# Kernel optimization log

Measured on AMD Instinct MI355X. Metric: run time of the kernel, lower is better.

Reference implementation:

```python
import jax, jax.numpy as jnp
import numpy as np

B, N, E, D, L, NC = 64, 128, 1024, 256, 2, 7
BETA = 0.3  # args.diffloss
BIG = 1e30  # mask_logic constant (score - (1-adj)*1e30), as in torch source lineage


def setup_inputs():
    key = jax.random.key(0)
    ks = iter(jax.random.split(key, 48))
    def p(shape, s=0.02):
        return jax.random.normal(next(ks), shape, jnp.float32) * s
    inp = {}
    inp["features"] = jax.random.normal(next(ks), (B, N, E), jnp.float32)
    inp["adj_1"] = jax.random.randint(next(ks), (B, N, N), 0, 2, jnp.int32)
    inp["adj_2"] = jax.random.randint(next(ks), (B, N, N), 0, 2, jnp.int32)
    inp["s_mask"] = jax.random.randint(next(ks), (B, N, N), 0, 2, jnp.int32)
    inp["s_mask_onehot"] = jnp.zeros((B, N, N, 2), jnp.int32)
    inp["lengths"] = jnp.full((B,), N, jnp.int32)
    inp["fc1_w"] = p((D, E)); inp["fc1_b"] = jnp.zeros((D,), jnp.float32)
    # GRUCell params (torch layout: weight_ih (3D,D) order r,z,n)
    for nm in ["gcs", "gps", "gcl", "gpl"]:
        inp[nm + "_wih"] = p((L, 3 * D, D)); inp[nm + "_whh"] = p((L, 3 * D, D))
        inp[nm + "_bih"] = jnp.zeros((L, 3 * D), jnp.float32)
        inp[nm + "_bhh"] = jnp.zeros((L, 3 * D), jnp.float32)
    # GatDot params per layer: linear1 (Q proj), linear2 (K proj)
    for nm in ["gats", "gatl"]:
        inp[nm + "_wq"] = p((L, D, D)); inp[nm + "_bq"] = jnp.zeros((L, D), jnp.float32)
        inp[nm + "_wk"] = p((L, D, D)); inp[nm + "_bk"] = jnp.zeros((L, D), jnp.float32)
    inp["affine1"] = p((2 * D, 2 * D), 0.05)
    inp["affine2"] = p((2 * D, 2 * D), 0.05)
    IN = 4 * D + E  # hidden*2*2 + emb_dim
    inp["mlp_w1"] = p((D, IN)); inp["mlp_b1"] = jnp.zeros((D,), jnp.float32)
    inp["mlp_w2"] = p((D, D)); inp["mlp_b2"] = jnp.zeros((D,), jnp.float32)
    inp["out_w"] = p((NC, D)); inp["out_b"] = jnp.zeros((NC,), jnp.float32)
    return inp


def gru_cell(x, h, wih, whh, bih, bhh):
    gi = x @ wih.T + bih
    gh = h @ whh.T + bhh
    ir, iz, in_ = jnp.split(gi, 3, axis=-1)
    hr, hz, hn = jnp.split(gh, 3, axis=-1)
    r = jax.nn.sigmoid(ir + hr)
    z = jax.nn.sigmoid(iz + hz)
    n = jnp.tanh(in_ + r * hn)
    return (1.0 - z) * n + z * h


def dag_pass(H_in, adj, gat, cpar, ppar):
    """Sequential DAG pass: per-utterance masked dot-product gather + GRU-C/GRU-P."""
    wq, bq, wk, bk = gat
    n = H_in.shape[1]
    idx = jnp.arange(n)

    def step(carry, inp):
        H1, Kb = carry            # H1: [B,N,D] written prefix; Kb = linear2(H1)
        i, x, arow = inp          # x: [B,D], arow: [B,N]
        q = x @ wq.T + bq
        scores = jnp.einsum('bnd,bd->bn', Kb, q)
        # torch: alpha - (1-adj)*1e30 over prefix :i; positions >= i excluded
        logits = scores - (1.0 - arow) * BIG - (idx >= i).astype(scores.dtype) * (2.0 * BIG)
        w = jax.nn.softmax(logits, axis=-1)
        M = jnp.einsum('bn,bnd->bd', w, H1)  # exactly 0 at i==0 (buffer zeros)
        C = gru_cell(x, M, *cpar)   # grus_c(input=x, hidden=M)
        P = gru_cell(M, x, *ppar)   # grus_p(input=M, hidden=x)
        h = C + P
        H1 = jax.lax.dynamic_update_slice(H1, h[:, None, :], (0, i, 0))
        Kb = jax.lax.dynamic_update_slice(Kb, (h @ wk.T + bk)[:, None, :], (0, i, 0))
        return (H1, Kb), None

    init = (jnp.zeros_like(H_in), jnp.zeros_like(H_in))
    xs = (idx, jnp.swapaxes(H_in, 0, 1), jnp.swapaxes(adj, 0, 1))
    (H1, _), _ = jax.lax.scan(step, init, xs)
    return H1


def diff_loss_fn(a, b):
    # orthogonality (DSN-style) loss between short/long channel features
    x = a.reshape(-1, a.shape[-1])
    y = b.reshape(-1, b.shape[-1])
    x = x - x.mean(axis=0, keepdims=True)
    y = y - y.mean(axis=0, keepdims=True)
    x = x / (jnp.linalg.norm(x, axis=1, keepdims=True) + 1e-6)
    y = y / (jnp.linalg.norm(y, axis=1, keepdims=True) + 1e-6)
    return jnp.mean((x.T @ y) ** 2)


def _forward(features, adj_1, adj_2,
             fc1_w, fc1_b,
             gcs_wih, gcs_whh, gcs_bih, gcs_bhh,
             gps_wih, gps_whh, gps_bih, gps_bhh,
             gcl_wih, gcl_whh, gcl_bih, gcl_bhh,
             gpl_wih, gpl_whh, gpl_bih, gpl_bhh,
             gats_wq, gats_bq, gats_wk, gats_bk,
             gatl_wq, gatl_bq, gatl_wk, gatl_bk,
             affine1, affine2,
             mlp_w1, mlp_b1, mlp_w2, mlp_b2, out_w, out_b):
    adj1 = adj_1.astype(jnp.float32)
    adj2 = adj_2.astype(jnp.float32)
    H0 = jax.nn.relu(features @ fc1_w.T + fc1_b)
    H0r = jax.nn.relu(features[:, ::-1] @ fc1_w.T + fc1_b)
    adj1r = adj1[:, ::-1, ::-1]
    adj2r = adj2[:, ::-1, ::-1]

    def channel(adjf, adjb, wq, bq, wk, bk, cwih, cwhh, cbih, cbhh, pwih, pwhh, pbih, pbhh):
        Hf, Hb = H0, H0r
        outs = []
        for l in range(L):
            gat = (wq[l], bq[l], wk[l], bk[l])
            cp = (cwih[l], cwhh[l], cbih[l], cbhh[l])
            pp = (pwih[l], pwhh[l], pbih[l], pbhh[l])
            Hf = dag_pass(Hf, adjf, gat, cp, pp)
            Hb = dag_pass(Hb, adjb, gat, cp, pp)
            outs.append(jnp.concatenate([Hf, Hb], axis=-1))  # no flip-back (as in source)
        return outs

    cs = channel(adj1, adj1r, gats_wq, gats_bq, gats_wk, gats_bk,
                 gcs_wih, gcs_whh, gcs_bih, gcs_bhh, gps_wih, gps_whh, gps_bih, gps_bhh)
    cl = channel(adj2, adj2r, gatl_wq, gatl_bq, gatl_wk, gatl_bk,
                 gcl_wih, gcl_whh, gcl_bih, gcl_bhh, gpl_wih, gpl_whh, gpl_bih, gpl_bhh)

    dloss = sum(diff_loss_fn(a, b) for a, b in zip(cs, cl)) * BETA

    HS, HL = cs[-1], cl[-1]  # [B,N,2D]
    A1 = jax.nn.softmax(jnp.einsum('bnd,de,bme->bnm', HS, affine1, HL), axis=-1)
    A2 = jax.nn.softmax(jnp.einsum('bnd,de,bme->bnm', HL, affine2, HS), axis=-1)
    HSn = jnp.einsum('bnm,bmd->bnd', A1, HL)
    HLn = jnp.einsum('bnm,bmd->bnd', A2, HS)

    Hfin = jnp.concatenate([features, HSn, HLn], axis=-1)  # in_dim = emb + 4D
    h = jax.nn.relu(Hfin @ mlp_w1.T + mlp_b1)
    h = jax.nn.relu(h @ mlp_w2.T + mlp_b2)
    logits = h @ out_w.T + out_b
    return logits, dloss


def reference(features, adj_1, adj_2, s_mask, s_mask_onehot, lengths,
              fc1_w, fc1_b,
              gcs_wih, gcs_whh, gcs_bih, gcs_bhh,
              gps_wih, gps_whh, gps_bih, gps_bhh,
              gcl_wih, gcl_whh, gcl_bih, gcl_bhh,
              gpl_wih, gpl_whh, gpl_bih, gpl_bhh,
              gats_wq, gats_bq, gats_wk, gats_bk,
              gatl_wq, gatl_bq, gatl_wk, gatl_bk,
              affine1, affine2,
              mlp_w1, mlp_b1, mlp_w2, mlp_b2, out_w, out_b):
    # s_mask / s_mask_onehot / lengths unused for attn_type='dotprod', no_rel_attn=True, nodal_att_type=None
    return _forward(features, adj_1, adj_2,
                    fc1_w, fc1_b,
                    gcs_wih, gcs_whh, gcs_bih, gcs_bhh,
                    gps_wih, gps_whh, gps_bih, gps_bhh,
                    gcl_wih, gcl_whh, gcl_bih, gcl_bhh,
                    gpl_wih, gpl_whh, gpl_bih, gpl_bhh,
                    gats_wq, gats_bq, gats_wk, gats_bk,
                    gatl_wq, gatl_bq, gatl_wk, gatl_bk,
                    affine1, affine2,
                    mlp_w1, mlp_b1, mlp_w2, mlp_b2, out_w, out_b)
```

## Files before the change

### kernel.cpp

```cpp
#include <hip/hip_runtime.h>
#include <hip/hip_fp16.h>
#include <math.h>

#define SB   64
#define SN   128
#define SE   1024
#define SD   256
#define SD2  512
#define SD3  768
#define SIN  2048
#define SNC  7
#define SBN  8192
#define CS   16

#define L_HS   0
#define L_GK   65536
#define L_XH   114688
#define L_QH   122880
#define L_MH   131072
#define L_LG   131584
#define L_WGT  132096
#define L_ADJ  132608
#define SMEM_BYTES 133120

typedef _Float16 h2v __attribute__((ext_vector_type(2)));

__device__ __forceinline__ float wsum(float v){
#pragma unroll
  for (int o = 32; o; o >>= 1) v += __shfl_xor(v, o);
  return v;
}
__device__ __forceinline__ float sigm(float x){ return 1.f/(1.f + expf(-x)); }

__device__ __forceinline__ unsigned short f2h(float f){
  return __half_as_ushort(__float2half_rn(f));
}
__device__ __forceinline__ float h2f_(unsigned short u){
  return __half2float(__ushort_as_half(u));
}
__device__ __forceinline__ h2v u2h(unsigned u){
  union { unsigned u; h2v h; } c; c.u = u; return c.h;
}
__device__ __forceinline__ float dot8d(uint4 w, uint4 m, float acc){
  acc = __builtin_amdgcn_fdot2(u2h(w.x), u2h(m.x), acc, false);
  acc = __builtin_amdgcn_fdot2(u2h(w.y), u2h(m.y), acc, false);
  acc = __builtin_amdgcn_fdot2(u2h(w.z), u2h(m.z), acc, false);
  acc = __builtin_amdgcn_fdot2(u2h(w.w), u2h(m.w), acc, false);
  return acc;
}

template<bool BKMAJ, bool BIAS, bool RELU, bool ACC>
__global__ __launch_bounds__(256)
void gemm_k(const float* __restrict__ A, const float* __restrict__ Bm,
            const float* __restrict__ bias, float* __restrict__ C,
            int Nn, int K, int lda, int ldb, int ldc,
            long sA, long sB, long sC)
// ... 74 lines not shown
  for (int p = 0; p < 6; ++p) {
    const int r = t + 256 * p;
    const float* src = (r < 768) ? (a.wc[cd] + (long)r * SD)
                                 : (a.wp[cd] + (long)(r - 768) * SD);
    const float4 v0 = *(const float4*)(src + kb8 * 8);
    const float4 v1 = *(const float4*)(src + kb8 * 8 + 4);
    uint4 o;
    o.x = (unsigned)f2h(v0.x) | ((unsigned)f2h(v0.y) << 16);
    o.y = (unsigned)f2h(v0.z) | ((unsigned)f2h(v0.w) << 16);
    o.z = (unsigned)f2h(v1.x) | ((unsigned)f2h(v1.y) << 16);
    o.w = (unsigned)f2h(v1.z) | ((unsigned)f2h(v1.w) << 16);
    *(uint4*)(a.Wt + (((size_t)cd * 32 + kb8) * 1536 + r) * 8) = o;
  }
}

__global__ void s0_k(const float* __restrict__ Q, const float* __restrict__ bk,
                     float* __restrict__ S0)
{
  const int r = blockIdx.x * 4 + (threadIdx.x >> 6), lane = threadIdx.x & 63;
  const float4 q  = *(const float4*)(Q + (long)r * SD + lane * 4);
  const float4 kb = *(const float4*)(bk + lane * 4);
  float p = q.x*kb.x + q.y*kb.y + q.z*kb.z + q.w*kb.w;
  p = wsum(p);
  if (lane == 0) S0[r] = p;
}

struct StepArgs {
  const float* Qt[4]; const float* S0[4];
  const int* adj[4]; int rev[4];
  const float* bc[4];  const float* bp[4];
  const float* bgc[4]; const float* bgp[4];
  const float* X[4];
  float* H1[4];
  unsigned short* Hh;
  const unsigned short* Wt;
  const unsigned short* Wgk;
  int ldX, s0;
};
__global__ __launch_bounds__(256, 1) void step_chunk_k(StepArgs a)
{
  extern __shared__ __align__(16) char dsm[];
  unsigned short* Hs_l = (unsigned short*)(dsm + L_HS);
  unsigned short* GKh  = (unsigned short*)(dsm + L_GK);
  unsigned short* Xh   = (unsigned short*)(dsm + L_XH);
  unsigned short* Qh   = (unsigned short*)(dsm + L_QH);
  unsigned short* Mh   = (unsigned short*)(dsm + L_MH);
  float* lg   = (float*)(dsm + L_LG);
  float* wgt  = (float*)(dsm + L_WGT);
  float* adjm = (float*)(dsm + L_ADJ);

  const int blk = blockIdx.x;
  const int cd = blk & 3, b = blk >> 2;
  const int t = threadIdx.x, q = t >> 6, l = t & 63;
  const int j = t;
  const int ldX = a.ldX, s0 = a.s0;
  const float* Xp  = a.X[cd];
  float* H1 = a.H1[cd];
  unsigned short* Hg = a.Hh + ((size_t)(cd * 64 + b)) * 128 * 256;
  const float* Qtp = a.Qt[cd];
  const float* S0p = a.S0[cd];
  const int*   adjp = a.adj[cd];
  const int    rev  = a.rev[cd];

  const float bc0 = a.bc[cd][j],  bc1 = a.bc[cd][256+j],  bc2 = a.bc[cd][512+j];
  const float bp0 = a.bp[cd][j],  bp1 = a.bp[cd][256+j],  bp2 = a.bp[cd][512+j];

#pragma unroll
  for (int s = 0; s < CS; ++s) {
    Xh[s*256 + t] = f2h(Xp[((long)(s0+s)*64 + b)*ldX + t]);
    Qh[s*256 + t] = f2h(Qtp[((long)(s0+s)*64 + b)*SD + t]);
  }
  for (int o = t*16; o < s0*512; o += 4096) {
    const uint4 v = *(const uint4*)((const char*)Hg + o);
    const int row = o >> 9, d2 = o & 511;
    *(uint4*)((char*)Hs_l + row*512 + (d2 ^ ((row & 7) << 4))) = v;
  }
  __syncthreads();

  {
    float gacc[6][CS];
#pragma unroll
    for (int g = 0; g < 6; ++g)
#pragma unroll
      for (int s = 0; s < CS; ++s) gacc[g][s] = 0.f;
    const unsigned short* wbase = a.Wgk + ((size_t)cd*32*1536 + j)*8;
    for (int kb8 = 0; kb8 < 32; ++kb8) {
      const uint4* wr = (const uint4*)(wbase + (size_t)kb8*12288);
      uint4 w[6];
#pragma unroll
      for (int g = 0; g < 6; ++g) w[g] = wr[g*256];
#pragma unroll
      for (int s = 0; s < CS; ++s) {
        const uint4 x8 = *(const uint4*)&Xh[s*256 + kb8*8];
#pragma unroll
        for (int g = 0; g < 6; ++g)
          gacc[g][s] = dot8d(w[g], x8, gacc[g][s]);
      }
    }
#pragma unroll
    for (int g = 0; g < 6; ++g) {
      const float bg = (g < 3) ? a.bgc[cd][g*256 + j] : a.bgp[cd][(g-3)*256 + j];
#pragma unroll
      for (int s = 0; s < CS; ++s)
        GKh[s*1536 + g*256 + j] = f2h(gacc[g][s] + bg);
    }
  }
  __syncthreads();

  for (int i = s0; i < s0 + CS; ++i) {
    float mreg;
    if (i == 0) {
      Mh[t] = 0;
      mreg = 0.f;
      __syncthreads();
    } else {
      if (t >= 128) {
        const int r = t - 128;
        const int ii = rev ? (SN-1-i) : i;
        const int nn = rev ? (SN-1-r) : r;
        adjm[r] = (float)adjp[((long)b*SN + ii)*SN + nn];
      } else {
        const int n = q*64 + l;
        const char* hrow = (const char*)Hs_l + n*512;
        const int c = (n & 7) << 4;
        const unsigned short* qrow = Qh + (i - s0)*256;
        float acc = 0.f;
#pragma unroll
        for (int k = 0; k < 32; ++k) {
          const uint4 hv = *(const uint4*)(hrow + ((k*16) ^ c));
          const uint4 qv = *(const uint4*)(qrow + k*8);
          acc = dot8d(hv, qv, acc);
        }
        lg[n] = acc;
      }
      __syncthreads();
      if (q == 0) {
        const float s0v = S0p[i*64 + b];
        const float v0 = (l < i)    ? (lg[l]    + s0v - (1.f - adjm[l]   )*1e30f) : -3.0e38f;
        const float v1 = (l+64 < i) ? (lg[l+64] + s0v - (1.f - adjm[l+64])*1e30f) : -3.0e38f;
        float mx = fmaxf(v0, v1);
#pragma unroll
        for (int o = 32; o; o >>= 1) mx = fmaxf(mx, __shfl_xor(mx, o));
        const float e0 = (l < i)    ? expf(v0 - mx) : 0.f;
        const float e1 = (l+64 < i) ? expf(v1 - mx) : 0.f;
        float sum = e0 + e1;
#pragma unroll
        for (int o = 32; o; o >>= 1) sum += __shfl_xor(sum, o);
        const float inv = 1.f / sum;
        if (l < i)    wgt[l]    = e0 * inv;
        if (l+64 < i) wgt[l+64] = e1 * inv;
      }
      __syncthreads();
      float m0 = 0.f, m1 = 0.f, m2 = 0.f, m3 = 0.f;
      int n = 0;
      for (; n + 8 <= i; n += 8) {
        m0 = fmaf(wgt[n+0], h2f_(Hs_l[(n+0)*256 + (j ^  0)]), m0);
        m1 = fmaf(wgt[n+1], h2f_(Hs_l[(n+1)*256 + (j ^  8)]), m1);
        m2 = fmaf(wgt[n+2], h2f_(Hs_l[(n+2)*256 + (j ^ 16)]), m2);
        m3 = fmaf(wgt[n+3], h2f_(Hs_l[(n+3)*256 + (j ^ 24)]), m3);
        m0 = fmaf(wgt[n+4], h2f_(Hs_l[(n+4)*256 + (j ^ 32)]), m0);
        m1 = fmaf(wgt[n+5], h2f_(Hs_l[(n+5)*256 + (j ^ 40)]), m1);
        m2 = fmaf(wgt[n+6], h2f_(Hs_l[(n+6)*256 + (j ^ 48)]), m2);
        m3 = fmaf(wgt[n+7], h2f_(Hs_l[(n+7)*256 + (j ^ 56)]), m3);
      }
      for (; n < i; ++n)
        m0 = fmaf(wgt[n], h2f_(Hs_l[n*256 + (j ^ ((n & 7) << 3))]), m0);
      mreg = (m0 + m1) + (m2 + m3);
      Mh[t] = f2h(mreg);
      __syncthreads();
    }

    float g0 = 0.f, g1 = 0.f, g2 = 0.f, g3 = 0.f, g4 = 0.f, g5 = 0.f;
    {
      const unsigned short* wb = a.Wt + ((size_t)cd*32*1536 + j)*8;
      const uint4* wr0 = (const uint4*)wb;
      uint4 c0 = wr0[0], c1 = wr0[256], c2 = wr0[512],
            c3 = wr0[768], c4 = wr0[1024], c5 = wr0[1280];
#pragma unroll 4
      for (int kb8 = 0; kb8 < 32; ++kb8) {
        uint4 n0 = c0, n1 = c1, n2 = c2, n3 = c3, n4 = c4, n5 = c5;
        if (kb8 < 31) {
          const uint4* wn = (const uint4*)(wb + (size_t)(kb8+1)*12288);
          n0 = wn[0]; n1 = wn[256]; n2 = wn[512];
          n3 = wn[768]; n4 = wn[1024]; n5 = wn[1280];
        }
        const uint4 m8 = *(const uint4*)&Mh[kb8*8];
        g0 = dot8d(c0, m8, g0);
        g1 = dot8d(c1, m8, g1);
        g2 = dot8d(c2, m8, g2);
        g3 = dot8d(c3, m8, g3);
        g4 = dot8d(c4, m8, g4);
        g5 = dot8d(c5, m8, g5);
        c0 = n0; c1 = n1; c2 = n2; c3 = n3; c4 = n4; c5 = n5;
      }
    }
    {
      const int sb = (i - s0)*1536;
      const float gic_r = h2f_(GKh[sb + j]);
      const float gic_z = h2f_(GKh[sb + 256 + j]);
      const float gic_n = h2f_(GKh[sb + 512 + j]);
      const float ghp_r = h2f_(GKh[sb + 768 + j]);
      const float ghp_z = h2f_(GKh[sb + 1024 + j]);
      const float ghp_n = h2f_(GKh[sb + 1280 + j]);
      const float xj = Xp[((long)i*64 + b)*ldX + j];
      const float rC = sigm(gic_r + g0 + bc0);
      const float zC = sigm(gic_z + g1 + bc1);
      const float nC = tanhf(gic_n + rC * (g2 + bc2));
      const float Cc = (1.f - zC) * nC + zC * mreg;
      const float rP = sigm(g3 + bp0 + ghp_r);
      const float zP = sigm(g4 + bp1 + ghp_z);
      const float nP = tanhf(g5 + bp2 + rP * ghp_n);
      const float hval = Cc + (1.f - zP) * nP + zP * xj;
      H1[((long)i*64 + b)*SD2 + j] = hval;
      const unsigned short hh = f2h(hval);
      Hs_l[i*256 + (j ^ ((i & 7) << 3))] = hh;
      Hg[(size_t)i*256 + j] = hh;
    }
    __syncthreads();
  }
}

__global__ void zero_k(float* p, long n)
{
  for (long idx = (long)blockIdx.x * 256 + threadIdx.x; idx < n; idx += (long)gridDim.x * 256)
    p[idx] = 0.f;
}

__global__ void colmean_k(const float* __restrict__ X, float* __restrict__ mean)
{
  __shared__ float red[256];
  const int c = blockIdx.x * 64 + (threadIdx.x & 63), rq = threadIdx.x >> 6;
  const int r0 = blockIdx.y * 256;
  float acc = 0.f;
  for (int r = r0 + rq; r < r0 + 256; r += 4) acc += X[(long)r * SD2 + c];
  red[threadIdx.x] = acc;
  __syncthreads();
  if (threadIdx.x < 64) {
    const float s = red[threadIdx.x] + red[64 + threadIdx.x] + red[128 + threadIdx.x] + red[192 + threadIdx.x];
    atomicAdd(&mean[c], s * (1.f / 8192.f));
  }
}

__global__ void rownorm_k(const float* __restrict__ X, const float* __restrict__ mean,
                          float* __restrict__ inv)
{
  const int r = blockIdx.x * 4 + (threadIdx.x >> 6), lane = threadIdx.x & 63;
  const float* xp = X + (long)r * SD2 + lane * 8;
  const float4 v0 = *(const float4*)xp;
  const float4 v1 = *(const float4*)(xp + 4);
  const float4 m0 = *(const float4*)(mean + lane * 8);
  const float4 m1 = *(const float4*)(mean + lane * 8 + 4);
// ... 83 lines not shown
#pragma unroll
  for (int o = 32; o; o >>= 1) s += __shfl_xor(s, o);
  const float inv = 1.f / s;
  p[lane] = e0 * inv; p[lane + 64] = e1 * inv;
}

__global__ void head_k(const float* __restrict__ H, const float* __restrict__ W,
                       const float* __restrict__ bo, float* __restrict__ out)
{
  const int r = blockIdx.x * 4 + (threadIdx.x >> 6), lane = threadIdx.x & 63;
  const float4 h = *(const float4*)(H + (long)r * SD + lane * 4);
#pragma unroll
  for (int c = 0; c < SNC; ++c) {
    const float4 w = *(const float4*)(W + (long)c * SD + lane * 4);
    float p = h.x*w.x + h.y*w.y + h.z*w.z + h.w*w.w;
    p = wsum(p);
    if (lane == 0) out[(long)r * SNC + c] = p + bo[c];
  }
}

__global__ void fin_k(const float* __restrict__ dl, float* __restrict__ out)
{
  out[0] = (dl[0] + dl[1]) * (0.3f / (512.f * 512.f));
}

extern "C" void kernel_launch(void* const* d_in, const int* in_sizes, int n_in,
                              void* d_out, int out_size, void* d_ws, size_t ws_size,
                              hipStream_t stream)
{
  (void)in_sizes; (void)n_in; (void)out_size; (void)ws_size;

  static bool attr_set = false;
  if (!attr_set) {
    hipFuncSetAttribute(reinterpret_cast<const void*>(step_chunk_k),
                        hipFuncAttributeMaxDynamicSharedMemorySize, SMEM_BYTES);
    attr_set = true;
  }

  const float* F    = (const float*)d_in[0];
  const int*   adj1 = (const int*)  d_in[1];
  const int*   adj2 = (const int*)  d_in[2];
  const float* fc1w = (const float*)d_in[6];
  const float* fc1b = (const float*)d_in[7];
  const float *g_wih[4], *g_whh[4], *g_bih[4], *g_bhh[4];
  for (int g = 0; g < 4; ++g) {
    g_wih[g] = (const float*)d_in[8 + g*4 + 0];
    g_whh[g] = (const float*)d_in[8 + g*4 + 1];
    g_bih[g] = (const float*)d_in[8 + g*4 + 2];
    g_bhh[g] = (const float*)d_in[8 + g*4 + 3];
  }
  const float* gat_wq[2] = {(const float*)d_in[24], (const float*)d_in[28]};
  const float* gat_bq[2] = {(const float*)d_in[25], (const float*)d_in[29]};
  const float* gat_wk[2] = {(const float*)d_in[26], (const float*)d_in[30]};
  const float* gat_bk[2] = {(const float*)d_in[27], (const float*)d_in[31]};
  const float* aff1 = (const float*)d_in[32];
  const float* aff2 = (const float*)d_in[33];
  const float* mw1  = (const float*)d_in[34];
  const float* mb1  = (const float*)d_in[35];
  const float* mw2  = (const float*)d_in[36];
  const float* mb2  = (const float*)d_in[37];
  const float* ow   = (const float*)d_in[38];
  const float* ob   = (const float*)d_in[39];
  float* out = (float*)d_out;

  float* ws = (float*)d_ws;
  size_t off = 0;
  auto take = [&](size_t nf){ float* p = ws + off; off += nf; return p; };
  float* region = take(22552576);
  float* X0f  = region;
  float* X0r  = region + 2097152;
  float* Qtb  = region + 4194304;
  float* Qtmp = region + 12582912;
  float* Htmp = region + 14680064;
  float* T  = region;
  float* Sb = region + 4194304;
  float* HH = region + 5242880;
  float* h1 = region + 9437184;
  float* h2 = region + 11534336;
  float* Ocat[2][2];
  for (int c = 0; c < 2; ++c) for (int l = 0; l < 2; ++l) Ocat[c][l] = take(4194304);
  float* S0b   = take(32768);
  unsigned short* WtB  = (unsigned short*)take(786432);
  unsigned short* WgkB = (unsigned short*)take(786432);
  unsigned short* HhB  = (unsigned short*)take(4194304);
  float* meanx = take(512);
  float* meany = take(512);
  float* invx  = take(8192);
  float* invy  = take(8192);
  float* dl    = take(8);
  float* Gbuf  = take(262144);

  gemm_k<false,true,true,false><<<dim3(4,64,1),256,0,stream>>>(
      F, fc1w, fc1b, Htmp, SD, SE, SE, SE, SD, 0,0,0);
  spread_k<<<SBN,256,0,stream>>>(Htmp, X0f, X0r);

  for (int l = 0; l < 2; ++l) {
    PTArgs pt, pg; StepArgs sta;
    sta.ldX = l ? SD2 : SD;
    sta.Wt = WtB; sta.Wgk = WgkB; sta.Hh = HhB;
    const int ldX = sta.ldX;
    for (int cd = 0; cd < 4; ++cd) {
      const int ch = cd >> 1;
      const float* X = (l == 0) ? ((cd & 1) ? X0r : X0f)
                                : (Ocat[ch][0] + (cd & 1) * SD);
      const float* wq   = gat_wq[ch] + l * SD * SD;
      const float* bq   = gat_bq[ch] + l * SD;
      const float* wk   = gat_wk[ch] + l * SD * SD;
      const float* bk   = gat_bk[ch] + l * SD;
      const float* cwih = g_wih[ch*2+0] + l * SD3 * SD;
      const float* cwhh = g_whh[ch*2+0] + l * SD3 * SD;
      const float* cbih = g_bih[ch*2+0] + l * SD3;
      const float* cbhh = g_bhh[ch*2+0] + l * SD3;
      const float* pwih = g_wih[ch*2+1] + l * SD3 * SD;
      const float* pwhh = g_whh[ch*2+1] + l * SD3 * SD;
      const float* pbih = g_bih[ch*2+1] + l * SD3;
      const float* pbhh = g_bhh[ch*2+1] + l * SD3;
      pt.wc[cd] = cwhh; pt.wp[cd] = pwih;
      pg.wc[cd] = cwih; pg.wp[cd] = pwhh;
      gemm_k<false,true,false,false><<<dim3(4,64,1),256,0,stream>>>(
          X, wq, bq, Qtmp, SD, SD, ldX, SD, SD, 0,0,0);
      gemm_k<true,false,false,false><<<dim3(4,64,1),256,0,stream>>>(
          Qtmp, wk, nullptr, Qtb + (size_t)cd*2097152, SD, SD, SD, SD, SD, 0,0,0);
      s0_k<<<SBN/4,256,0,stream>>>(Qtmp, bk, S0b + cd*SBN);
      float* H1mut = Ocat[ch][l] + (cd & 1) * SD;
      sta.Qt[cd] = Qtb + (size_t)cd*2097152;
      sta.S0[cd] = S0b + cd*SBN;
      sta.H1[cd] = H1mut;
      sta.adj[cd] = ch ? adj2 : adj1; sta.rev[cd] = cd & 1;
      sta.bc[cd]  = cbhh; sta.bp[cd]  = pbih;
      sta.bgc[cd] = cbih; sta.bgp[cd] = pbhh;
      sta.X[cd] = X;
    }
    pt.Wt = WtB;  packT_k<<<dim3(32,4),256,0,stream>>>(pt);
    pg.Wt = WgkB; packT_k<<<dim3(32,4),256,0,stream>>>(pg);

    for (int s0 = 0; s0 < SN; s0 += CS) {
      sta.s0 = s0;
      step_chunk_k<<<256,256,SMEM_BYTES,stream>>>(sta);
    }
  }

  zero_k<<<1,256,0,stream>>>(dl, 2);
  for (int l = 0; l < 2; ++l) {
    zero_k<<<4,256,0,stream>>>(meanx, 1024);
    colmean_k<<<dim3(8,32,1),256,0,stream>>>(Ocat[0][l], meanx);
    colmean_k<<<dim3(8,32,1),256,0,stream>>>(Ocat[1][l], meany);
    rownorm_k<<<SBN/4,256,0,stream>>>(Ocat[0][l], meanx, invx);
    rownorm_k<<<SBN/4,256,0,stream>>>(Ocat[1][l], meany, invy);
    zero_k<<<256,256,0,stream>>>(Gbuf, (long)SD2*SD2);
    gpart_k<<<dim3(8,8,16),256,0,stream>>>(Ocat[0][l], Ocat[1][l], meanx, meany, invx, invy, Gbuf);
    sqsum_k<<<256,256,0,stream>>>(Gbuf, dl + l);
  }

  gemm_k<true,false,false,false><<<dim3(8,64,1),256,0,stream>>>(
      Ocat[0][1], aff1, nullptr, T, SD2, SD2, SD2, SD2, SD2, 0,0,0);
  gemm_k<false,false,false,false><<<dim3(2,1,64),256,0,stream>>>(
      T, Ocat[1][1], nullptr, Sb, SN, SD2, 64*SD2, 64*SD2, SN, SD2, SD2, (long)SN*SN);
  smax_k<<<SBN/4,256,0,stream>>>(Sb);
  gemm_k<true,false,false,false><<<dim3(8,1,64),256,0,stream>>>(
      Sb, Ocat[1][1], nullptr, HH, SD2, SN, SN, 64*SD2, SD2, (long)SN*SN, SD2, (long)SN*SD2);
  gemm_k<false,true,false,false><<<dim3(4,64,1),256,0,stream>>>(
      F, mw1, mb1, h1, SD, SE, SE, SIN, SD, 0,0,0);
  gemm_k<false,false,false,true><<<dim3(4,64,1),256,0,stream>>>(
      HH, mw1 + 1024, nullptr, h1, SD, SD2, SD2, SIN, SD, 0,0,0);
  gemm_k<true,false,false,false><<<dim3(8,64,1),256,0,stream>>>(
      Ocat[1][1], aff2, nullptr, T, SD2, SD2, SD2, SD2, SD2, 0,0,0);
  gemm_k<false,false,false,false><<<dim3(2,1,64),256,0,stream>>>(
      T, Ocat[0][1], nullptr, Sb, SN, SD2, 64*SD2, 64*SD2, SN, SD2, SD2, (long)SN*SN);
  smax_k<<<SBN/4,256,0,stream>>>(Sb);
  gemm_k<true,false,false,false><<<dim3(8,1,64),256,0,stream>>>(
      Sb, Ocat[0][1], nullptr, HH, SD2, SN, SN, 64*SD2, SD2, (long)SN*SN, SD2, (long)SN*SD2);
  gemm_k<false,false,true,true><<<dim3(4,64,1),256,0,stream>>>(
// ... 7 lines not shown
```

Measured before the change: 4.711 ms.

## Fuse per-chunk step launches into one persistent per-layer kernel

Replaces the eight per-chunk step kernel launches per layer with a single kernel that loops over all chunks and keeps the hidden-state history resident in LDS. This removes the global fp16 H history buffer along with its per-launch reload and per-step store. The change also prefetches the recurrent weights for each step before the attention phase, using four register buffers to hide latency, and preloads adjacency and S0 per chunk. It widens the LDS swizzle from 8 to 32 rows and skips logit computation for rows not yet reached. The main risk is higher register pressure from holding 24 uint4 weight registers plus the 96 gacc accumulators.

```diff
diff --git a/kernel.cpp b/kernel.cpp
--- a/kernel.cpp
+++ b/kernel.cpp
@@ -17,11 +17,12 @@
 #define L_GK   65536
 #define L_XH   114688
 #define L_QH   122880
-#define L_MH   131072
-#define L_LG   131584
-#define L_WGT  132096
-#define L_ADJ  132608
-#define SMEM_BYTES 133120
+#define L_ADJ  131072
+#define L_MH   139264
+#define L_LG   139776
+#define L_WGT  140288
+#define L_S0   140800
+#define SMEM_BYTES 140864
 
 typedef _Float16 h2v __attribute__((ext_vector_type(2)));
 
@@ -162,31 +163,29 @@
   const float* bgc[4]; const float* bgp[4];
   const float* X[4];
   float* H1[4];
-  unsigned short* Hh;
   const unsigned short* Wt;
   const unsigned short* Wgk;
-  int ldX, s0;
+  int ldX;
 };
-__global__ __launch_bounds__(256, 1) void step_chunk_k(StepArgs a)
+__global__ __launch_bounds__(256, 1) void step_layer_k(StepArgs a)
 {
   extern __shared__ __align__(16) char dsm[];
-  unsigned short* Hs_l = (unsigned short*)(dsm + L_HS);
-  unsigned short* GKh  = (unsigned short*)(dsm + L_GK);
-  unsigned short* Xh   = (unsigned short*)(dsm + L_XH);
-  unsigned short* Qh   = (unsigned short*)(dsm + L_QH);
-  unsigned short* Mh   = (unsigned short*)(dsm + L_MH);
+  unsigned short* Hs  = (unsigned short*)(dsm + L_HS);
+  unsigned short* GKh = (unsigned short*)(dsm + L_GK);
+  unsigned short* Xh  = (unsigned short*)(dsm + L_XH);
+  unsigned short* Qh  = (unsigned short*)(dsm + L_QH);
+  float* adjc = (float*)(dsm + L_ADJ);
+  unsigned short* Mh  = (unsigned short*)(dsm + L_MH);
   float* lg   = (float*)(dsm + L_LG);
   float* wgt  = (float*)(dsm + L_WGT);
-  float* adjm = (float*)(dsm + L_ADJ);
+  float* s0s  = (float*)(dsm + L_S0);
 
   const int blk = blockIdx.x;
   const int cd = blk & 3, b = blk >> 2;
-  const int t = threadIdx.x, q = t >> 6, l = t & 63;
-  const int j = t;
-  const int ldX = a.ldX, s0 = a.s0;
+  const int t = threadIdx.x, j = t;
+  const int ldX = a.ldX;
   const float* Xp  = a.X[cd];
   float* H1 = a.H1[cd];
-  unsigned short* Hg = a.Hh + ((size_t)(cd * 64 + b)) * 128 * 256;
   const float* Qtp = a.Qt[cd];
   const float* S0p = a.S0[cd];
   const int*   adjp = a.adj[cd];
@@ -194,159 +193,210 @@
 
   const float bc0 = a.bc[cd][j],  bc1 = a.bc[cd][256+j],  bc2 = a.bc[cd][512+j];
   const float bp0 = a.bp[cd][j],  bp1 = a.bp[cd][256+j],  bp2 = a.bp[cd][512+j];
-
-#pragma unroll
-  for (int s = 0; s < CS; ++s) {
-    Xh[s*256 + t] = f2h(Xp[((long)(s0+s)*64 + b)*ldX + t]);
-    Qh[s*256 + t] = f2h(Qtp[((long)(s0+s)*64 + b)*SD + t]);
-  }
-  for (int o = t*16; o < s0*512; o += 4096) {
-    const uint4 v = *(const uint4*)((const char*)Hg + o);
-    const int row = o >> 9, d2 = o & 511;
-    *(uint4*)((char*)Hs_l + row*512 + (d2 ^ ((row & 7) << 4))) = v;
-  }
-  __syncthreads();
-
-  {
-    float gacc[6][CS];
-#pragma unroll
-    for (int g = 0; g < 6; ++g)
-#pragma unroll
-      for (int s = 0; s < CS; ++s) gacc[g][s] = 0.f;
-    const unsigned short* wbase = a.Wgk + ((size_t)cd*32*1536 + j)*8;
-    for (int kb8 = 0; kb8 < 32; ++kb8) {
-      const uint4* wr = (const uint4*)(wbase + (size_t)kb8*12288);
-      uint4 w[6];
-#pragma unroll
-      for (int g = 0; g < 6; ++g) w[g] = wr[g*256];
-#pragma unroll
-      for (int s = 0; s < CS; ++s) {
-        const uint4 x8 = *(const uint4*)&Xh[s*256 + kb8*8];
-#pragma unroll
-        for (int g = 0; g < 6; ++g)
-          gacc[g][s] = dot8d(w[g], x8, gacc[g][s]);
-      }
-    }
-#pragma unroll
-    for (int g = 0; g < 6; ++g) {
-      const float bg = (g < 3) ? a.bgc[cd][g*256 + j] : a.bgp[cd][(g-3)*256 + j];
-#pragma unroll
-      for (int s = 0; s < CS; ++s)
-        GKh[s*1536 + g*256 + j] = f2h(gacc[g][s] + bg);
-    }
-  }
-  __syncthreads();
-
-  for (int i = s0; i < s0 + CS; ++i) {
-    float mreg;
-    if (i == 0) {
-      Mh[t] = 0;
-      mreg = 0.f;
+  const unsigned short* wb   = a.Wt  + ((size_t)cd*32*1536 + j)*8;
+  const unsigned short* wbgk = a.Wgk + ((size_t)cd*32*1536 + j)*8;
+
+  for (int c0 = 0; c0 < SN; c0 += CS) {
+    __syncthreads();
+#pragma unroll
+    for (int s = 0; s < CS; ++s) {
+      Xh[s*256 + t] = f2h(Xp[((long)(c0+s)*64 + b)*ldX + t]);
+      Qh[s*256 + t] = f2h(Qtp[((long)(c0+s)*64 + b)*SD + t]);
+    }
+    for (int z = t; z < CS*128; z += 256) {
+      const int s = z >> 7, n = z & 127;
+      const int i = c0 + s;
+      int av = 0;
+      if (i > 0) {
+        const int ii = rev ? (SN-1-i) : i;
+        const int nn = rev ? (SN-1-n) : n;
+        av = adjp[((long)b*SN + ii)*SN + nn];
+      }
+      adjc[z] = (float)av;
+    }
+    if (t < CS) s0s[t] = S0p[(c0+t)*64 + b];
+    __syncthreads();
+
+    {
+      float gacc[6][CS];
+#pragma unroll
+      for (int g = 0; g < 6; ++g)
+#pragma unroll
+        for (int s = 0; s < CS; ++s) gacc[g][s] = 0.f;
+      uint4 wA[6], wB[6];
+#pragma unroll
+      for (int g = 0; g < 6; ++g) {
+        wA[g] = ((const uint4*)wbgk)[g*256];
+        wB[g] = ((const uint4*)(wbgk + 12288))[g*256];
+      }
+      for (int kb8 = 0; kb8 < 32; kb8 += 2) {
+#pragma unroll
+        for (int s = 0; s < CS; ++s) {
+          const uint4 x8 = *(const uint4*)&Xh[s*256 + kb8*8];
+#pragma unroll
+          for (int g = 0; g < 6; ++g) gacc[g][s] = dot8d(wA[g], x8, gacc[g][s]);
+        }
+        if (kb8 + 2 < 32) {
+          const uint4* wr = (const uint4*)(wbgk + (size_t)(kb8+2)*12288);
+#pragma unroll
+          for (int g = 0; g < 6; ++g) wA[g] = wr[g*256];
+        }
+#pragma unroll
+        for (int s = 0; s < CS; ++s) {
+          const uint4 x8 = *(const uint4*)&Xh[s*256 + kb8*8 + 8];
+#pragma unroll
+          for (int g = 0; g < 6; ++g) gacc[g][s] = dot8d(wB[g], x8, gacc[g][s]);
+        }
+        if (kb8 + 3 < 32) {
+          const uint4* wr = (const uint4*)(wbgk + (size_t)(kb8+3)*12288);
+#pragma unroll
+          for (int g = 0; g < 6; ++g) wB[g] = wr[g*256];
+        }
+      }
+#pragma unroll
+      for (int g = 0; g < 6; ++g) {
+        const float bg = (g < 3) ? a.bgc[cd][g*256 + j] : a.bgp[cd][(g-3)*256 + j];
+#pragma unroll
+        for (int s = 0; s < CS; ++s)
+          GKh[s*1536 + g*256 + j] = f2h(gacc[g][s] + bg);
+      }
+    }
+    __syncthreads();
+
+    for (int s = 0; s < CS; ++s) {
+      const int i = c0 + s;
+      const float xj = Xp[((long)i*64 + b)*ldX + j];
+      uint4 wA[6], wB[6], wC[6], wD[6];
+#pragma unroll
+      for (int g = 0; g < 6; ++g) {
+        wA[g] = ((const uint4*)wb)[g*256];
+        wB[g] = ((const uint4*)(wb + 12288))[g*256];
+        wC[g] = ((const uint4*)(wb + 24576))[g*256];
+        wD[g] = ((const uint4*)(wb + 36864))[g*256];
+      }
+      float mreg;
+      if (i == 0) {
+        Mh[t] = 0;
+        mreg = 0.f;
+        __syncthreads();
+      } else {
+        if (t < 128 && (t & 64) < i) {
+          const int n = t;
+          const char* hrow = (const char*)Hs + n*512;
+          const int cx = (n & 31) << 4;
+          const unsigned short* qrow = Qh + s*256;
+          float acc = 0.f;
+#pragma unroll
+          for (int k = 0; k < 32; ++k) {
+            const uint4 hv = *(const uint4*)(hrow + ((k*16) ^ cx));
+            const uint4 qv = *(const uint4*)(qrow + k*8);
+            acc = dot8d(hv, qv, acc);
+          }
+          lg[n] = acc;
+        }
+        __syncthreads();
+        if (t < 64) {
+          const float s0v = s0s[s];
+          const int l = t;
+          const float v0 = (l < i)    ? (lg[l]    + s0v - (1.f - adjc[s*128+l]   )*1e30f) : -3.0e38f;
+          const float v1 = (l+64 < i) ? (lg[l+64] + s0v - (1.f - adjc[s*128+l+64])*1e30f) : -3.0e38f;
+          float mx = fmaxf(v0, v1);
+#pragma unroll
+          for (int o = 32; o; o >>= 1) mx = fmaxf(mx, __shfl_xor(mx, o));
+          const float e0 = (l < i)    ? expf(v0 - mx) : 0.f;
+          const float e1 = (l+64 < i) ? expf(v1 - mx) : 0.f;
+          float sum = e0 + e1;
+#pragma unroll
+          for (int o = 32; o; o >>= 1) sum += __shfl_xor(sum, o);
+          const float inv = 1.f / sum;
+          if (l < i)    wgt[l]    = e0 * inv;
+          if (l+64 < i) wgt[l+64] = e1 * inv;
+        }
+        __syncthreads();
+        float m0 = 0.f, m1 = 0.f, m2 = 0.f, m3 = 0.f;
+        int n = 0;
+        for (; n + 4 <= i; n += 4) {
+          m0 = fmaf(wgt[n+0], h2f_(Hs[(n+0)*256 + (j ^ (((n+0)&31)<<3))]), m0);
+          m1 = fmaf(wgt[n+1], h2f_(Hs[(n+1)*256 + (j ^ (((n+1)&31)<<3))]), m1);
+          m2 = fmaf(wgt[n+2], h2f_(Hs[(n+2)*256 + (j ^ (((n+2)&31)<<3))]), m2);
+          m3 = fmaf(wgt[n+3], h2f_(Hs[(n+3)*256 + (j ^ (((n+3)&31)<<3))]), m3);
+        }
+        for (; n < i; ++n)
+          m0 = fmaf(wgt[n], h2f_(Hs[n*256 + (j ^ ((n&31)<<3))]), m0);
+        mreg = (m0 + m1) + (m2 + m3);
+        Mh[t] = f2h(mreg);
+        __syncthreads();
+      }
+
+      float g0 = 0.f, g1 = 0.f, g2 = 0.f, g3 = 0.f, g4 = 0.f, g5 = 0.f;
+      for (int kb = 0; kb < 32; kb += 4) {
+        {
+          const uint4 m8 = *(const uint4*)&Mh[kb*8];
+          g0 = dot8d(wA[0], m8, g0); g1 = dot8d(wA[1], m8, g1);
+          g2 = dot8d(wA[2], m8, g2); g3 = dot8d(wA[3], m8, g3);
+          g4 = dot8d(wA[4], m8, g4); g5 = dot8d(wA[5], m8, g5);
+        }
+        if (kb < 28) {
+          const uint4* w = (const uint4*)(wb + (size_t)(kb+4)*12288);
+#pragma unroll
+          for (int g = 0; g < 6; ++g) wA[g] = w[g*256];
+        }
+        {
+          const uint4 m8 = *(const uint4*)&Mh[kb*8 + 8];
+          g0 = dot8d(wB[0], m8, g0); g1 = dot8d(wB[1], m8, g1);
+          g2 = dot8d(wB[2], m8, g2); g3 = dot8d(wB[3], m8, g3);
+          g4 = dot8d(wB[4], m8, g4); g5 = dot8d(wB[5], m8, g5);
+        }
+        if (kb < 28) {
+          const uint4* w = (const uint4*)(wb + (size_t)(kb+5)*12288);
+#pragma unroll
+          for (int g = 0; g < 6; ++g) wB[g] = w[g*256];
+        }
+        {
+          const uint4 m8 = *(const uint4*)&Mh[kb*8 + 16];
+          g0 = dot8d(wC[0], m8, g0); g1 = dot8d(wC[1], m8, g1);
+          g2 = dot8d(wC[2], m8, g2); g3 = dot8d(wC[3], m8, g3);
+          g4 = dot8d(wC[4], m8, g4); g5 = dot8d(wC[5], m8, g5);
+        }
+        if (kb < 28) {
+          const uint4* w = (const uint4*)(wb + (size_t)(kb+6)*12288);
+#pragma unroll
+          for (int g = 0; g < 6; ++g) wC[g] = w[g*256];
+        }
+        {
+          const uint4 m8 = *(const uint4*)&Mh[kb*8 + 24];
+          g0 = dot8d(wD[0], m8, g0); g1 = dot8d(wD[1], m8, g1);
+          g2 = dot8d(wD[2], m8, g2); g3 = dot8d(wD[3], m8, g3);
+          g4 = dot8d(wD[4], m8, g4); g5 = dot8d(wD[5], m8, g5);
+        }
+        if (kb < 28) {
+          const uint4* w = (const uint4*)(wb + (size_t)(kb+7)*12288);
+#pragma unroll
+          for (int g = 0; g < 6; ++g) wD[g] = w[g*256];
+        }
+      }
+
+      {
+        const int sb = s*1536;
+        const float gic_r = h2f_(GKh[sb + j]);
+        const float gic_z = h2f_(GKh[sb + 256 + j]);
+        const float gic_n = h2f_(GKh[sb + 512 + j]);
+        const float ghp_r = h2f_(GKh[sb + 768 + j]);
+        const float ghp_z = h2f_(GKh[sb + 1024 + j]);
+        const float ghp_n = h2f_(GKh[sb + 1280 + j]);
+        const float rC = sigm(gic_r + g0 + bc0);
+        const float zC = sigm(gic_z + g1 + bc1);
+        const float nC = tanhf(gic_n + rC * (g2 + bc2));
+        const float Cc = (1.f - zC) * nC + zC * mreg;
+        const float rP = sigm(g3 + bp0 + ghp_r);
+        const float zP = sigm(g4 + bp1 + ghp_z);
+        const float nP = tanhf(g5 + bp2 + rP * ghp_n);
+        const float hval = Cc + (1.f - zP) * nP + zP * xj;
+        H1[((long)i*64 + b)*SD2 + j] = hval;
+        Hs[i*256 + (j ^ ((i & 31) << 3))] = f2h(hval);
+      }
       __syncthreads();
-    } else {
-      if (t >= 128) {
-        const int r = t - 128;
-        const int ii = rev ? (SN-1-i) : i;
-        const int nn = rev ? (SN-1-r) : r;
-        adjm[r] = (float)adjp[((long)b*SN + ii)*SN + nn];
-      } else {
-        const int n = q*64 + l;
-        const char* hrow = (const char*)Hs_l + n*512;
-        const int c = (n & 7) << 4;
-        const unsigned short* qrow = Qh + (i - s0)*256;
-        float acc = 0.f;
-#pragma unroll
-        for (int k = 0; k < 32; ++k) {
-          const uint4 hv = *(const uint4*)(hrow + ((k*16) ^ c));
-          const uint4 qv = *(const uint4*)(qrow + k*8);
-          acc = dot8d(hv, qv, acc);
-        }
-        lg[n] = acc;
-      }
-      __syncthreads();
-      if (q == 0) {
-        const float s0v = S0p[i*64 + b];
-        const float v0 = (l < i)    ? (lg[l]    + s0v - (1.f - adjm[l]   )*1e30f) : -3.0e38f;
-        const float v1 = (l+64 < i) ? (lg[l+64] + s0v - (1.f - adjm[l+64])*1e30f) : -3.0e38f;
-        float mx = fmaxf(v0, v1);
-#pragma unroll
-        for (int o = 32; o; o >>= 1) mx = fmaxf(mx, __shfl_xor(mx, o));
-        const float e0 = (l < i)    ? expf(v0 - mx) : 0.f;
-        const float e1 = (l+64 < i) ? expf(v1 - mx) : 0.f;
-        float sum = e0 + e1;
-#pragma unroll
-        for (int o = 32; o; o >>= 1) sum += __shfl_xor(sum, o);
-        const float inv = 1.f / sum;
-        if (l < i)    wgt[l]    = e0 * inv;
-        if (l+64 < i) wgt[l+64] = e1 * inv;
-      }
-      __syncthreads();
-      float m0 = 0.f, m1 = 0.f, m2 = 0.f, m3 = 0.f;
-      int n = 0;
-      for (; n + 8 <= i; n += 8) {
-        m0 = fmaf(wgt[n+0], h2f_(Hs_l[(n+0)*256 + (j ^  0)]), m0);
-        m1 = fmaf(wgt[n+1], h2f_(Hs_l[(n+1)*256 + (j ^  8)]), m1);
-        m2 = fmaf(wgt[n+2], h2f_(Hs_l[(n+2)*256 + (j ^ 16)]), m2);
-        m3 = fmaf(wgt[n+3], h2f_(Hs_l[(n+3)*256 + (j ^ 24)]), m3);
-        m0 = fmaf(wgt[n+4], h2f_(Hs_l[(n+4)*256 + (j ^ 32)]), m0);
-        m1 = fmaf(wgt[n+5], h2f_(Hs_l[(n+5)*256 + (j ^ 40)]), m1);
-        m2 = fmaf(wgt[n+6], h2f_(Hs_l[(n+6)*256 + (j ^ 48)]), m2);
-        m3 = fmaf(wgt[n+7], h2f_(Hs_l[(n+7)*256 + (j ^ 56)]), m3);
-      }
-      for (; n < i; ++n)
-        m0 = fmaf(wgt[n], h2f_(Hs_l[n*256 + (j ^ ((n & 7) << 3))]), m0);
-      mreg = (m0 + m1) + (m2 + m3);
-      Mh[t] = f2h(mreg);
-      __syncthreads();
-    }
-
-    float g0 = 0.f, g1 = 0.f, g2 = 0.f, g3 = 0.f, g4 = 0.f, g5 = 0.f;
-    {
-      const unsigned short* wb = a.Wt + ((size_t)cd*32*1536 + j)*8;
-      const uint4* wr0 = (const uint4*)wb;
-      uint4 c0 = wr0[0], c1 = wr0[256], c2 = wr0[512],
-            c3 = wr0[768], c4 = wr0[1024], c5 = wr0[1280];
-#pragma unroll 4
-      for (int kb8 = 0; kb8 < 32; ++kb8) {
-        uint4 n0 = c0, n1 = c1, n2 = c2, n3 = c3, n4 = c4, n5 = c5;
-        if (kb8 < 31) {
-          const uint4* wn = (const uint4*)(wb + (size_t)(kb8+1)*12288);
-          n0 = wn[0]; n1 = wn[256]; n2 = wn[512];
-          n3 = wn[768]; n4 = wn[1024]; n5 = wn[1280];
-        }
-        const uint4 m8 = *(const uint4*)&Mh[kb8*8];
-        g0 = dot8d(c0, m8, g0);
-        g1 = dot8d(c1, m8, g1);
-        g2 = dot8d(c2, m8, g2);
-        g3 = dot8d(c3, m8, g3);
-        g4 = dot8d(c4, m8, g4);
-        g5 = dot8d(c5, m8, g5);
-        c0 = n0; c1 = n1; c2 = n2; c3 = n3; c4 = n4; c5 = n5;
-      }
-    }
-    {
-      const int sb = (i - s0)*1536;
-      const float gic_r = h2f_(GKh[sb + j]);
-      const float gic_z = h2f_(GKh[sb + 256 + j]);
-      const float gic_n = h2f_(GKh[sb + 512 + j]);
-      const float ghp_r = h2f_(GKh[sb + 768 + j]);
-      const float ghp_z = h2f_(GKh[sb + 1024 + j]);
-      const float ghp_n = h2f_(GKh[sb + 1280 + j]);
-      const float xj = Xp[((long)i*64 + b)*ldX + j];
-      const float rC = sigm(gic_r + g0 + bc0);
-      const float zC = sigm(gic_z + g1 + bc1);
-      const float nC = tanhf(gic_n + rC * (g2 + bc2));
-      const float Cc = (1.f - zC) * nC + zC * mreg;
-      const float rP = sigm(g3 + bp0 + ghp_r);
-      const float zP = sigm(g4 + bp1 + ghp_z);
-      const float nP = tanhf(g5 + bp2 + rP * ghp_n);
-      const float hval = Cc + (1.f - zP) * nP + zP * xj;
-      H1[((long)i*64 + b)*SD2 + j] = hval;
-      const unsigned short hh = f2h(hval);
-      Hs_l[i*256 + (j ^ ((i & 7) << 3))] = hh;
-      Hg[(size_t)i*256 + j] = hh;
-    }
-    __syncthreads();
+    }
   }
 }
 
@@ -496,7 +546,7 @@
 
   static bool attr_set = false;
   if (!attr_set) {
-    hipFuncSetAttribute(reinterpret_cast<const void*>(step_chunk_k),
+    hipFuncSetAttribute(reinterpret_cast<const void*>(step_layer_k),
                         hipFuncAttributeMaxDynamicSharedMemorySize, SMEM_BYTES);
     attr_set = true;
   }
@@ -546,7 +596,6 @@
   float* S0b   = take(32768);
   unsigned short* WtB  = (unsigned short*)take(786432);
   unsigned short* WgkB = (unsigned short*)take(786432);
-  unsigned short* HhB  = (unsigned short*)take(4194304);
   float* meanx = take(512);
   float* meany = take(512);
   float* invx  = take(8192);
@@ -561,7 +610,7 @@
   for (int l = 0; l < 2; ++l) {
     PTArgs pt, pg; StepArgs sta;
     sta.ldX = l ? SD2 : SD;
-    sta.Wt = WtB; sta.Wgk = WgkB; sta.Hh = HhB;
+    sta.Wt = WtB; sta.Wgk = WgkB;
     const int ldX = sta.ldX;
     for (int cd = 0; cd < 4; ++cd) {
       const int ch = cd >> 1;
@@ -598,10 +647,7 @@
     pt.Wt = WtB;  packT_k<<<dim3(32,4),256,0,stream>>>(pt);
     pg.Wt = WgkB; packT_k<<<dim3(32,4),256,0,stream>>>(pg);
 
-    for (int s0 = 0; s0 < SN; s0 += CS) {
-      sta.s0 = s0;
-      step_chunk_k<<<256,256,SMEM_BYTES,stream>>>(sta);
-    }
+    step_layer_k<<<256,256,SMEM_BYTES,stream>>>(sta);
   }
 
   zero_k<<<1,256,0,stream>>>(dl, 2);
```

Measured after the change: 5.586 ms. +18.6%, slower.

## Split logit dot across all threads, prefetch adjacency per chunk, widen LDS swizzle

Applied to the files above, without the earlier changes.

The per-step logit computation now uses all 256 threads, each doing half of a 256-wide dot product, and the two partial sums are added in the softmax warp. Rows at or beyond the current step are skipped. The adjacency rows and S0 values for the whole 16-step chunk are preloaded into LDS at chunk start, which takes the global adjacency load off the sequential critical path. The H swizzle widens from 8 to 32 rows to cut bank conflicts, and the gather loop unroll drops from 8 to 4. This costs more LDS and an extra partial-sum read.

```diff
diff --git a/kernel.cpp b/kernel.cpp
--- a/kernel.cpp
+++ b/kernel.cpp
@@ -17,11 +17,12 @@
 #define L_GK   65536
 #define L_XH   114688
 #define L_QH   122880
-#define L_MH   131072
-#define L_LG   131584
-#define L_WGT  132096
-#define L_ADJ  132608
-#define SMEM_BYTES 133120
+#define L_ADJ  131072
+#define L_MH   139264
+#define L_LGP  139776
+#define L_WGT  140800
+#define L_S0   141312
+#define SMEM_BYTES 141376
 
 typedef _Float16 h2v __attribute__((ext_vector_type(2)));
 
@@ -170,20 +171,20 @@
 __global__ __launch_bounds__(256, 1) void step_chunk_k(StepArgs a)
 {
   extern __shared__ __align__(16) char dsm[];
-  unsigned short* Hs_l = (unsigned short*)(dsm + L_HS);
-  unsigned short* GKh  = (unsigned short*)(dsm + L_GK);
-  unsigned short* Xh   = (unsigned short*)(dsm + L_XH);
-  unsigned short* Qh   = (unsigned short*)(dsm + L_QH);
-  unsigned short* Mh   = (unsigned short*)(dsm + L_MH);
-  float* lg   = (float*)(dsm + L_LG);
+  unsigned short* Hs  = (unsigned short*)(dsm + L_HS);
+  unsigned short* GKh = (unsigned short*)(dsm + L_GK);
+  unsigned short* Xh  = (unsigned short*)(dsm + L_XH);
+  unsigned short* Qh  = (unsigned short*)(dsm + L_QH);
+  float* adjc = (float*)(dsm + L_ADJ);
+  unsigned short* Mh  = (unsigned short*)(dsm + L_MH);
+  float* lgp  = (float*)(dsm + L_LGP);
   float* wgt  = (float*)(dsm + L_WGT);
-  float* adjm = (float*)(dsm + L_ADJ);
+  float* s0s  = (float*)(dsm + L_S0);
 
   const int blk = blockIdx.x;
   const int cd = blk & 3, b = blk >> 2;
-  const int t = threadIdx.x, q = t >> 6, l = t & 63;
-  const int j = t;
-  const int ldX = a.ldX, s0 = a.s0;
+  const int t = threadIdx.x, j = t;
+  const int ldX = a.ldX, c0 = a.s0;
   const float* Xp  = a.X[cd];
   float* H1 = a.H1[cd];
   unsigned short* Hg = a.Hh + ((size_t)(cd * 64 + b)) * 128 * 256;
@@ -197,13 +198,25 @@
 
 #pragma unroll
   for (int s = 0; s < CS; ++s) {
-    Xh[s*256 + t] = f2h(Xp[((long)(s0+s)*64 + b)*ldX + t]);
-    Qh[s*256 + t] = f2h(Qtp[((long)(s0+s)*64 + b)*SD + t]);
-  }
-  for (int o = t*16; o < s0*512; o += 4096) {
+    Xh[s*256 + t] = f2h(Xp[((long)(c0+s)*64 + b)*ldX + t]);
+    Qh[s*256 + t] = f2h(Qtp[((long)(c0+s)*64 + b)*SD + t]);
+  }
+  for (int z = t; z < CS*128; z += 256) {
+    const int s = z >> 7, n = z & 127;
+    const int i = c0 + s;
+    int av = 0;
+    if (i > 0) {
+      const int ii = rev ? (SN-1-i) : i;
+      const int nn = rev ? (SN-1-n) : n;
+      av = adjp[((long)b*SN + ii)*SN + nn];
+    }
+    adjc[z] = (float)av;
+  }
+  if (t < CS) s0s[t] = S0p[(c0+t)*64 + b];
+  for (int o = t*16; o < c0*512; o += 4096) {
     const uint4 v = *(const uint4*)((const char*)Hg + o);
     const int row = o >> 9, d2 = o & 511;
-    *(uint4*)((char*)Hs_l + row*512 + (d2 ^ ((row & 7) << 4))) = v;
+    *(uint4*)((char*)Hs + row*512 + (d2 ^ ((row & 31) << 4))) = v;
   }
   __syncthreads();
 
@@ -237,37 +250,37 @@
   }
   __syncthreads();
 
-  for (int i = s0; i < s0 + CS; ++i) {
-    float mreg;
+  for (int s = 0; s < CS; ++s) {
+    const int i = c0 + s;
+    float mreg = 0.f;
     if (i == 0) {
       Mh[t] = 0;
-      mreg = 0.f;
       __syncthreads();
     } else {
-      if (t >= 128) {
-        const int r = t - 128;
-        const int ii = rev ? (SN-1-i) : i;
-        const int nn = rev ? (SN-1-r) : r;
-        adjm[r] = (float)adjp[((long)b*SN + ii)*SN + nn];
-      } else {
-        const int n = q*64 + l;
-        const char* hrow = (const char*)Hs_l + n*512;
-        const int c = (n & 7) << 4;
-        const unsigned short* qrow = Qh + (i - s0)*256;
-        float acc = 0.f;
-#pragma unroll
-        for (int k = 0; k < 32; ++k) {
-          const uint4 hv = *(const uint4*)(hrow + ((k*16) ^ c));
-          const uint4 qv = *(const uint4*)(qrow + k*8);
-          acc = dot8d(hv, qv, acc);
+      {
+        const int n = t & 127, hi = t >> 7;
+        if (n < i) {
+          const char* hrow = (const char*)Hs + n*512;
+          const int cx = (n & 31) << 4;
+          const unsigned short* qrow = Qh + s*256 + hi*128;
+          float acc = 0.f;
+#pragma unroll
+          for (int k = 0; k < 16; ++k) {
+            const uint4 hv = *(const uint4*)(hrow + (((hi*16 + k)*16) ^ cx));
+            const uint4 qv = *(const uint4*)(qrow + k*8);
+            acc = dot8d(hv, qv, acc);
+          }
+          lgp[t] = acc;
         }
-        lg[n] = acc;
       }
       __syncthreads();
-      if (q == 0) {
-        const float s0v = S0p[i*64 + b];
-        const float v0 = (l < i)    ? (lg[l]    + s0v - (1.f - adjm[l]   )*1e30f) : -3.0e38f;
-        const float v1 = (l+64 < i) ? (lg[l+64] + s0v - (1.f - adjm[l+64])*1e30f) : -3.0e38f;
+      if (t < 64) {
+        const float s0v = s0s[s];
+        const int l = t;
+        const float lg0 = lgp[l]      + lgp[128 + l];
+        const float lg1 = lgp[64 + l] + lgp[192 + l];
+        const float v0 = (l < i)    ? (lg0 + s0v - (1.f - adjc[s*128+l]   )*1e30f) : -3.0e38f;
+        const float v1 = (l+64 < i) ? (lg1 + s0v - (1.f - adjc[s*128+l+64])*1e30f) : -3.0e38f;
         float mx = fmaxf(v0, v1);
 #pragma unroll
         for (int o = 32; o; o >>= 1) mx = fmaxf(mx, __shfl_xor(mx, o));
@@ -281,22 +294,20 @@
         if (l+64 < i) wgt[l+64] = e1 * inv;
       }
       __syncthreads();
-      float m0 = 0.f, m1 = 0.f, m2 = 0.f, m3 = 0.f;
-      int n = 0;
-      for (; n + 8 <= i; n += 8) {
-        m0 = fmaf(wgt[n+0], h2f_(Hs_l[(n+0)*256 + (j ^  0)]), m0);
-        m1 = fmaf(wgt[n+1], h2f_(Hs_l[(n+1)*256 + (j ^  8)]), m1);
-        m2 = fmaf(wgt[n+2], h2f_(Hs_l[(n+2)*256 + (j ^ 16)]), m2);
-        m3 = fmaf(wgt[n+3], h2f_(Hs_l[(n+3)*256 + (j ^ 24)]), m3);
-        m0 = fmaf(wgt[n+4], h2f_(Hs_l[(n+4)*256 + (j ^ 32)]), m0);
-        m1 = fmaf(wgt[n+5], h2f_(Hs_l[(n+5)*256 + (j ^ 40)]), m1);
-        m2 = fmaf(wgt[n+6], h2f_(Hs_l[(n+6)*256 + (j ^ 48)]), m2);
-        m3 = fmaf(wgt[n+7], h2f_(Hs_l[(n+7)*256 + (j ^ 56)]), m3);
+      {
+        float m0 = 0.f, m1 = 0.f, m2 = 0.f, m3 = 0.f;
+        int n = 0;
+        for (; n + 4 <= i; n += 4) {
+          m0 = fmaf(wgt[n+0], h2f_(Hs[(n+0)*256 + (j ^ (((n+0)&31)<<3))]), m0);
+          m1 = fmaf(wgt[n+1], h2f_(Hs[(n+1)*256 + (j ^ (((n+1)&31)<<3))]), m1);
+          m2 = fmaf(wgt[n+2], h2f_(Hs[(n+2)*256 + (j ^ (((n+2)&31)<<3))]), m2);
+          m3 = fmaf(wgt[n+3], h2f_(Hs[(n+3)*256 + (j ^ (((n+3)&31)<<3))]), m3);
+        }
+        for (; n < i; ++n)
+          m0 = fmaf(wgt[n], h2f_(Hs[n*256 + (j ^ ((n&31)<<3))]), m0);
+        mreg = (m0 + m1) + (m2 + m3);
+        Mh[t] = f2h(mreg);
       }
-      for (; n < i; ++n)
-        m0 = fmaf(wgt[n], h2f_(Hs_l[n*256 + (j ^ ((n & 7) << 3))]), m0);
-      mreg = (m0 + m1) + (m2 + m3);
-      Mh[t] = f2h(mreg);
       __syncthreads();
     }
 
@@ -304,28 +315,28 @@
     {
       const unsigned short* wb = a.Wt + ((size_t)cd*32*1536 + j)*8;
       const uint4* wr0 = (const uint4*)wb;
-      uint4 c0 = wr0[0], c1 = wr0[256], c2 = wr0[512],
-            c3 = wr0[768], c4 = wr0[1024], c5 = wr0[1280];
+      uint4 c0r = wr0[0], c1r = wr0[256], c2r = wr0[512],
+            c3r = wr0[768], c4r = wr0[1024], c5r = wr0[1280];
 #pragma unroll 4
       for (int kb8 = 0; kb8 < 32; ++kb8) {
-        uint4 n0 = c0, n1 = c1, n2 = c2, n3 = c3, n4 = c4, n5 = c5;
+        uint4 n0 = c0r, n1 = c1r, n2 = c2r, n3 = c3r, n4 = c4r, n5 = c5r;
         if (kb8 < 31) {
           const uint4* wn = (const uint4*)(wb + (size_t)(kb8+1)*12288);
           n0 = wn[0]; n1 = wn[256]; n2 = wn[512];
           n3 = wn[768]; n4 = wn[1024]; n5 = wn[1280];
         }
         const uint4 m8 = *(const uint4*)&Mh[kb8*8];
-        g0 = dot8d(c0, m8, g0);
-        g1 = dot8d(c1, m8, g1);
-        g2 = dot8d(c2, m8, g2);
-        g3 = dot8d(c3, m8, g3);
-        g4 = dot8d(c4, m8, g4);
-        g5 = dot8d(c5, m8, g5);
-        c0 = n0; c1 = n1; c2 = n2; c3 = n3; c4 = n4; c5 = n5;
+        g0 = dot8d(c0r, m8, g0);
+        g1 = dot8d(c1r, m8, g1);
+        g2 = dot8d(c2r, m8, g2);
+        g3 = dot8d(c3r, m8, g3);
+        g4 = dot8d(c4r, m8, g4);
+        g5 = dot8d(c5r, m8, g5);
+        c0r = n0; c1r = n1; c2r = n2; c3r = n3; c4r = n4; c5r = n5;
       }
     }
     {
-      const int sb = (i - s0)*1536;
+      const int sb = s*1536;
       const float gic_r = h2f_(GKh[sb + j]);
       const float gic_z = h2f_(GKh[sb + 256 + j]);
       const float gic_n = h2f_(GKh[sb + 512 + j]);
@@ -343,7 +354,7 @@
       const float hval = Cc + (1.f - zP) * nP + zP * xj;
       H1[((long)i*64 + b)*SD2 + j] = hval;
       const unsigned short hh = f2h(hval);
-      Hs_l[i*256 + (j ^ ((i & 7) << 3))] = hh;
+      Hs[i*256 + (j ^ ((i & 31) << 3))] = hh;
       Hg[(size_t)i*256 + j] = hh;
     }
     __syncthreads();
```

After: 4.743 ms. Within noise of the previous version (+0.7%).
